# Kernel tuning notes

Measured on AMD Instinct MI355X. Metric: run time of the kernel, lower is better.

## Reference

```python
import jax, jax.numpy as jnp
import numpy as np

D_MODEL = 1024
NUM_HEADS = 16
DEPTH = D_MODEL // NUM_HEADS
B, S = 2, 2048


def setup_inputs() -> dict:
    key = jax.random.key(0)
    ks = jax.random.split(key, 12)
    s = 1.0 / np.sqrt(D_MODEL)
    return {
        "query": jax.random.normal(ks[0], (B, S, D_MODEL), jnp.float32),
        "key": jax.random.normal(ks[1], (B, S, D_MODEL), jnp.float32),
        "value": jax.random.normal(ks[2], (B, S, D_MODEL), jnp.float32),
        "mask": jax.random.randint(ks[3], (B, S), 0, 2, jnp.int32),
        "Wq": jax.random.normal(ks[4], (D_MODEL, D_MODEL), jnp.float32) * s,
        "bq": jnp.zeros((D_MODEL,), jnp.float32),
        "Wk": jax.random.normal(ks[5], (D_MODEL, D_MODEL), jnp.float32) * s,
        "bk": jnp.zeros((D_MODEL,), jnp.float32),
        "Wv": jax.random.normal(ks[6], (D_MODEL, D_MODEL), jnp.float32) * s,
        "bv": jnp.zeros((D_MODEL,), jnp.float32),
        "Wo": jax.random.normal(ks[7], (D_MODEL, D_MODEL), jnp.float32) * s,
        "bo": jnp.zeros((D_MODEL,), jnp.float32),
    }


def _split_heads(x):
    # [B, S, D] -> [B, H, S, depth]
    b, s, _ = x.shape
    return x.reshape(b, s, NUM_HEADS, DEPTH).transpose(0, 2, 1, 3)


def reference(query, key, value, mask, Wq, bq, Wk, bk, Wv, bv, Wo, bo):
    q = _split_heads(query @ Wq.T + bq)
    k = _split_heads(key @ Wk.T + bk)
    v = _split_heads(value @ Wv.T + bv)
    scale = 1.0 / jnp.sqrt(jnp.float32(DEPTH))
    # [B, H, Sq, Sk]
    logits = jnp.einsum("bhqd,bhkd->bhqk", q, k) * scale
    logits = logits + mask.astype(logits.dtype)[:, None, None, :] * (-1e9)
    attn = jax.nn.softmax(logits, axis=-1)
    out = jnp.einsum("bhqk,bhkd->bhqd", attn, v)
    out = out.transpose(0, 2, 1, 3).reshape(query.shape[0], -1, D_MODEL)
    return out @ Wo.T + bo
```

## Files before the change

### kernel.cpp

```cpp
#include <hip/hip_runtime.h>

typedef _Float16 half8 __attribute__((ext_vector_type(8)));
typedef float floatx4 __attribute__((ext_vector_type(4)));

#define D_MODEL 1024
#define NHEAD   16
#define DH      64
#define BATCH   2
#define SEQ     2048
#define M_TOT   4096

#define GLD_LDS16(g, l)                                                          \
  __builtin_amdgcn_global_load_lds(                                              \
      (const __attribute__((address_space(1))) void*)(g),                        \
      (__attribute__((address_space(3))) void*)(l), 16, 0, 0)

__global__ __launch_bounds__(256) void cvt_all(const float* __restrict__ q,
                                               const float* __restrict__ k,
                                               const float* __restrict__ v,
                                               const float* __restrict__ wq,
                                               const float* __restrict__ wk,
                                               const float* __restrict__ wv,
                                               const float* __restrict__ wo,
                                               _Float16* __restrict__ Xall,
                                               _Float16* __restrict__ Wall) {
  int bid = blockIdx.x;
  const float* src;
  _Float16* dst;
  if (bid < 6144) {
    int tsr = bid >> 11;
    src = (tsr == 0) ? q : (tsr == 1) ? k : v;
    dst = Xall + (size_t)tsr * 4194304;
    bid &= 2047;
  } else {
    int w = (bid - 6144) >> 9;
    src = (w == 0) ? wq : (w == 1) ? wk : (w == 2) ? wv : wo;
    dst = Wall + (size_t)w * 1048576;
    bid = (bid - 6144) & 511;
  }
  int off = bid * 2048 + threadIdx.x * 8;
  float4 a = *(const float4*)(src + off);
  float4 b = *(const float4*)(src + off + 4);
  half8 h;
  h[0] = (_Float16)a.x; h[1] = (_Float16)a.y; h[2] = (_Float16)a.z; h[3] = (_Float16)a.w;
  h[4] = (_Float16)b.x; h[5] = (_Float16)b.y; h[6] = (_Float16)b.z; h[7] = (_Float16)b.w;
  *(half8*)(dst + off) = h;
}

__global__ __launch_bounds__(256) void gemm_qkv(const _Float16* __restrict__ Xall,
                                                const _Float16* __restrict__ Wall,
                                                const float* __restrict__ bq,
                                                const float* __restrict__ bk,
                                                const float* __restrict__ bv,
                                                _Float16* __restrict__ Obase) {
  __shared__ alignas(16) _Float16 As[128][32];
  __shared__ alignas(16) _Float16 Bs[128][32];

  const int z = blockIdx.z;
  const _Float16* X = Xall + (size_t)z * 4194304;
  const _Float16* W = Wall + (size_t)z * 1048576;
  const float* bias = (z == 0) ? bq : (z == 1) ? bk : bv;
  _Float16* out = Obase + (size_t)z * 4194304;

  const int t = threadIdx.x, lane = t & 63, wave = t >> 6;
  const int wr = wave >> 1, wc = wave & 1;
  const int m0 = blockIdx.y * 128, n0 = blockIdx.x * 128;
  const int fr = lane & 15, fc = (lane >> 4) * 8, rg = (lane >> 4) * 4;

  floatx4 acc[4][4];
  for (int i = 0; i < 4; i++)
    for (int j = 0; j < 4; j++) acc[i][j] = (floatx4){0.f, 0.f, 0.f, 0.f};

  const int srow = lane >> 2, scol = (lane & 3) * 8;
  const _Float16* gA0 = X + (size_t)(m0 + wave * 32 + srow) * 1024 + scol;
  const _Float16* gA1 = gA0 + 16 * 1024;
  const _Float16* gB0 = W + (size_t)(n0 + wave * 32 + srow) * 1024 + scol;
  const _Float16* gB1 = gB0 + 16 * 1024;
  _Float16* lA0 = &As[wave * 32][0];
  _Float16* lA1 = &As[wave * 32 + 16][0];
  _Float16* lB0 = &Bs[wave * 32][0];
  _Float16* lB1 = &Bs[wave * 32 + 16][0];

  for (int k0 = 0; k0 < 1024; k0 += 32) {
    GLD_LDS16(gA0 + k0, lA0);
    GLD_LDS16(gA1 + k0, lA1);
    GLD_LDS16(gB0 + k0, lB0);
    GLD_LDS16(gB1 + k0, lB1);
    __syncthreads();

    half8 af[4], bw[4];
    for (int i = 0; i < 4; i++) {
      af[i] = *(const half8*)&As[wr * 64 + i * 16 + fr][fc];
      bw[i] = *(const half8*)&Bs[wc * 64 + i * 16 + fr][fc];
    }
    for (int i = 0; i < 4; i++)
      for (int j = 0; j < 4; j++)
        acc[i][j] = __builtin_amdgcn_mfma_f32_16x16x32_f16(af[i], bw[j], acc[i][j], 0, 0, 0);
    __syncthreads();
  }

  for (int i = 0; i < 4; i++)
    for (int j = 0; j < 4; j++) {
      int n = n0 + wc * 64 + j * 16 + fr;
      float bv2 = bias[n];
      int hh = n >> 6, d = n & 63;
      for (int r = 0; r < 4; r++) {
        int m = m0 + wr * 64 + i * 16 + rg + r;
        int bb = m >> 11, s = m & 2047;
        out[(((size_t)(bb * NHEAD + hh)) * SEQ + s) * DH + d] =
            (_Float16)(acc[i][j][r] + bv2);
      }
    }
}

__global__ __launch_bounds__(256) void gemm_wo(const _Float16* __restrict__ ctx,
                                               const _Float16* __restrict__ W,
                                               const float* __restrict__ bias,
                                               float* __restrict__ out) {
  __shared__ alignas(16) _Float16 As[128][32];
  __shared__ alignas(16) _Float16 Bs[64][32];

  const int t = threadIdx.x, lane = t & 63, wave = t >> 6;
  const int m0 = blockIdx.y * 128, n0 = blockIdx.x * 64;
  const int fr = lane & 15, fc = (lane >> 4) * 8, rg = (lane >> 4) * 4;

  floatx4 acc[2][4];
  for (int i = 0; i < 2; i++)
    for (int j = 0; j < 4; j++) acc[i][j] = (floatx4){0.f, 0.f, 0.f, 0.f};

  const int srow = lane >> 2, scol = (lane & 3) * 8;
  const _Float16* gA0 = ctx + (size_t)(m0 + wave * 32 + srow) * 1024 + scol;
  const _Float16* gA1 = gA0 + 16 * 1024;
  const _Float16* gB0 = W + (size_t)(n0 + wave * 16 + srow) * 1024 + scol;
  _Float16* lA0 = &As[wave * 32][0];
  _Float16* lA1 = &As[wave * 32 + 16][0];
  _Float16* lB0 = &Bs[wave * 16][0];

  for (int k0 = 0; k0 < 1024; k0 += 32) {
    GLD_LDS16(gA0 + k0, lA0);
    GLD_LDS16(gA1 + k0, lA1);
    GLD_LDS16(gB0 + k0, lB0);
    __syncthreads();

    half8 af[2], bw[4];
    for (int i = 0; i < 2; i++)
      af[i] = *(const half8*)&As[wave * 32 + i * 16 + fr][fc];
    for (int j = 0; j < 4; j++)
      bw[j] = *(const half8*)&Bs[j * 16 + fr][fc];
    for (int i = 0; i < 2; i++)
      for (int j = 0; j < 4; j++)
        acc[i][j] = __builtin_amdgcn_mfma_f32_16x16x32_f16(af[i], bw[j], acc[i][j], 0, 0, 0);
    __syncthreads();
  }

  for (int i = 0; i < 2; i++)
    for (int j = 0; j < 4; j++) {
      int n = n0 + j * 16 + fr;
      float bv2 = bias[n];
      for (int r = 0; r < 4; r++) {
        int m = m0 + wave * 32 + i * 16 + rg + r;
        out[(size_t)m * D_MODEL + n] = acc[i][j][r] + bv2;
      }
    }
}

__global__ __launch_bounds__(256) void attn_kernel(const _Float16* __restrict__ Qp,
                                                   const _Float16* __restrict__ Kp,
                                                   const _Float16* __restrict__ Vp,
                                                   const int* __restrict__ mask,
                                                   _Float16* __restrict__ ctx) {
  __shared__ alignas(16) char lds[18432 + 34816 + 512];
  _Float16 (*Qs)[72]  = (_Float16(*)[72])lds;
  _Float16 (*Vt)[136] = (_Float16(*)[136])lds;
  _Float16 (*Ks)[72]  = (_Float16(*)[72])(lds + 18432);
  _Float16 (*Ps)[136] = (_Float16(*)[136])(lds + 18432);
  float* Ms = (float*)(lds + 18432 + 34816);

  const int b = blockIdx.z, h = blockIdx.y, q0 = blockIdx.x * 128;
  const int t = threadIdx.x, lane = t & 63, wave = t >> 6;
  const int fr = lane & 15, fc = (lane >> 4) * 8, rg = (lane >> 4) * 4;

  const _Float16* Qg = Qp + ((size_t)(b * NHEAD + h) * SEQ + q0) * DH;
  const _Float16* Kg = Kp + (size_t)(b * NHEAD + h) * SEQ * DH;
  const _Float16* Vg = Vp + (size_t)(b * NHEAD + h) * SEQ * DH;

  {
    int r = t >> 1, c0 = (t & 1) * 32;
    const half8* g = (const half8*)(Qg + r * 64 + c0);
    for (int u = 0; u < 4; u++)
      *(half8*)&Qs[r][c0 + u * 8] = g[u];
  }
  __syncthreads();
  half8 qf[2][2];
  for (int mi = 0; mi < 2; mi++)
    for (int kk = 0; kk < 2; kk++)
      qf[mi][kk] = *(const half8*)&Qs[wave * 32 + mi * 16 + fr][kk * 32 + fc];
  __syncthreads();

  float mrow[2][4], lrow[2][4];
  floatx4 oacc[2][4];
  for (int mi = 0; mi < 2; mi++)
    for (int r = 0; r < 4; r++) { mrow[mi][r] = -3.0e38f; lrow[mi][r] = 0.f; }
  for (int mi = 0; mi < 2; mi++)
    for (int dj = 0; dj < 4; dj++) oacc[mi][dj] = (floatx4){0.f, 0.f, 0.f, 0.f};

  for (int kt = 0; kt < SEQ / 128; kt++) {
    const int k0 = kt * 128;
    {
      int r = t >> 1, c0 = (t & 1) * 32;
      const half8* gk = (const half8*)(Kg + (k0 + r) * 64 + c0);
      for (int u = 0; u < 4; u++)
        *(half8*)&Ks[r][c0 + u * 8] = gk[u];
      const half8* gv = (const half8*)(Vg + (k0 + r) * 64 + c0);
      half8 vv[4];
      for (int u = 0; u < 4; u++) vv[u] = gv[u];
      for (int u = 0; u < 4; u++)
        for (int j = 0; j < 8; j++) Vt[c0 + u * 8 + j][r] = vv[u][j];
      if (t < 128) Ms[t] = (float)mask[b * SEQ + k0 + t] * -1.0e9f;
    }
    __syncthreads();

    floatx4 sa[2][8];
    for (int mi = 0; mi < 2; mi++)
      for (int nj = 0; nj < 8; nj++) sa[mi][nj] = (floatx4){0.f, 0.f, 0.f, 0.f};
    for (int nj = 0; nj < 8; nj++)
      for (int kk = 0; kk < 2; kk++) {
        half8 kf = *(const half8*)&Ks[nj * 16 + fr][kk * 32 + fc];
        sa[0][nj] = __builtin_amdgcn_mfma_f32_16x16x32_f16(qf[0][kk], kf, sa[0][nj], 0, 0, 0);
        sa[1][nj] = __builtin_amdgcn_mfma_f32_16x16x32_f16(qf[1][kk], kf, sa[1][nj], 0, 0, 0);
      }
    __syncthreads();

    for (int nj = 0; nj < 8; nj++) {
      float mk = Ms[nj * 16 + fr];
      for (int mi = 0; mi < 2; mi++)
        for (int r = 0; r < 4; r++)
          sa[mi][nj][r] = sa[mi][nj][r] * 0.125f + mk;
    }

    for (int mi = 0; mi < 2; mi++) {
      for (int r = 0; r < 4; r++) {
        float tm = sa[mi][0][r];
        for (int nj = 1; nj < 8; nj++) tm = fmaxf(tm, sa[mi][nj][r]);
        for (int off = 1; off < 16; off <<= 1) tm = fmaxf(tm, __shfl_xor(tm, off));
        float mnew = fmaxf(mrow[mi][r], tm);
        float alpha = __expf(mrow[mi][r] - mnew);
        mrow[mi][r] = mnew;
        float rs = 0.f;
        for (int nj = 0; nj < 8; nj++) {
          float p = __expf(sa[mi][nj][r] - mnew);
          sa[mi][nj][r] = p;
          rs += p;
        }
        for (int off = 1; off < 16; off <<= 1) rs += __shfl_xor(rs, off);
        lrow[mi][r] = lrow[mi][r] * alpha + rs;
        for (int dj = 0; dj < 4; dj++) oacc[mi][dj][r] *= alpha;
      }
    }

    for (int mi = 0; mi < 2; mi++)
      for (int nj = 0; nj < 8; nj++)
        for (int r = 0; r < 4; r++)
          Ps[wave * 32 + mi * 16 + rg + r][nj * 16 + fr] = (_Float16)sa[mi][nj][r];
    __syncthreads();

    for (int kk = 0; kk < 4; kk++) {
      half8 pf[2], vf[4];
      for (int mi = 0; mi < 2; mi++)
        pf[mi] = *(const half8*)&Ps[wave * 32 + mi * 16 + fr][kk * 32 + fc];
      for (int dj = 0; dj < 4; dj++)
        vf[dj] = *(const half8*)&Vt[dj * 16 + fr][kk * 32 + fc];
      for (int mi = 0; mi < 2; mi++)
        for (int dj = 0; dj < 4; dj++)
          oacc[mi][dj] = __builtin_amdgcn_mfma_f32_16x16x32_f16(pf[mi], vf[dj], oacc[mi][dj], 0, 0, 0);
    }
    __syncthreads();
  }

  for (int mi = 0; mi < 2; mi++)
    for (int r = 0; r < 4; r++) {
      float inv = 1.0f / lrow[mi][r];
      int qrow = q0 + wave * 32 + mi * 16 + rg + r;
      _Float16* o = ctx + ((size_t)b * SEQ + qrow) * D_MODEL + h * DH;
      for (int dj = 0; dj < 4; dj++)
        o[dj * 16 + fr] = (_Float16)(oacc[mi][dj][r] * inv);
    }
}

extern "C" void kernel_launch(void* const* d_in, const int* in_sizes, int n_in,
                              void* d_out, int out_size, void* d_ws, size_t ws_size,
                              hipStream_t stream) {
  const float* query = (const float*)d_in[0];
  const float* key   = (const float*)d_in[1];
  const float* value = (const float*)d_in[2];
  const int*   mask  = (const int*)d_in[3];
  const float* Wq = (const float*)d_in[4];
  const float* bq = (const float*)d_in[5];
  const float* Wk = (const float*)d_in[6];
  const float* bk = (const float*)d_in[7];
  const float* Wv = (const float*)d_in[8];
  const float* bv = (const float*)d_in[9];
  const float* Wo = (const float*)d_in[10];
  const float* bo = (const float*)d_in[11];

  char* ws = (char*)d_ws;
  _Float16* Xall = (_Float16*)(ws);
  _Float16* Wall = (_Float16*)(ws + (size_t)24 * 1024 * 1024);
  _Float16* Qp   = (_Float16*)(ws + (size_t)32 * 1024 * 1024);
  _Float16* ctx  = (_Float16*)(ws + (size_t)56 * 1024 * 1024);

  _Float16* Kp = Qp + (size_t)4194304;
  _Float16* Vp = Qp + (size_t)8388608;

  cvt_all<<<8192, 256, 0, stream>>>(query, key, value, Wq, Wk, Wv, Wo, Xall, Wall);

  gemm_qkv<<<dim3(8, 32, 3), 256, 0, stream>>>(Xall, Wall, bq, bk, bv, Qp);

  attn_kernel<<<dim3(SEQ / 128, NHEAD, BATCH), 256, 0, stream>>>(Qp, Kp, Vp, mask, ctx);

  gemm_wo<<<dim3(16, 32), 256, 0, stream>>>(ctx, Wall + (size_t)3 * 1048576, bo, (float*)d_out);
}
```

Before: 282.5 us.

## Write V pre-transposed from QKV GEMM and load Q fragments directly

The QKV GEMM epilogue for V now stages tiles in shared memory and writes V in a [B,H,DH,SEQ] transposed layout with vectorized stores. The attention kernel can then load V^T tiles with 16-byte copies instead of scattering elements into a transposed LDS tile on every key block. Q fragments are also read straight from global memory, which removes the Q staging buffer and two barriers. The cost is extra LDS traffic and barriers in the V GEMM epilogue.

```diff
diff --git a/kernel.cpp b/kernel.cpp
--- a/kernel.cpp
+++ b/kernel.cpp
@@ -53,8 +53,10 @@
                                                 const float* __restrict__ bk,
                                                 const float* __restrict__ bv,
                                                 _Float16* __restrict__ Obase) {
-  __shared__ alignas(16) _Float16 As[128][32];
-  __shared__ alignas(16) _Float16 Bs[128][32];
+  __shared__ alignas(16) char smem[17408];
+  _Float16 (*As)[32]  = (_Float16(*)[32])smem;
+  _Float16 (*Bs)[32]  = (_Float16(*)[32])(smem + 8192);
+  _Float16 (*Ts)[136] = (_Float16(*)[136])smem;
 
   const int z = blockIdx.z;
   const _Float16* X = Xall + (size_t)z * 4194304;
@@ -99,18 +101,40 @@
     __syncthreads();
   }
 
-  for (int i = 0; i < 4; i++)
-    for (int j = 0; j < 4; j++) {
-      int n = n0 + wc * 64 + j * 16 + fr;
-      float bv2 = bias[n];
-      int hh = n >> 6, d = n & 63;
-      for (int r = 0; r < 4; r++) {
-        int m = m0 + wr * 64 + i * 16 + rg + r;
-        int bb = m >> 11, s = m & 2047;
-        out[(((size_t)(bb * NHEAD + hh)) * SEQ + s) * DH + d] =
-            (_Float16)(acc[i][j][r] + bv2);
-      }
-    }
+  if (z != 2) {
+    for (int i = 0; i < 4; i++)
+      for (int j = 0; j < 4; j++) {
+        int n = n0 + wc * 64 + j * 16 + fr;
+        float bv2 = bias[n];
+        int hh = n >> 6, d = n & 63;
+        for (int r = 0; r < 4; r++) {
+          int m = m0 + wr * 64 + i * 16 + rg + r;
+          int bb = m >> 11, s = m & 2047;
+          out[(((size_t)(bb * NHEAD + hh)) * SEQ + s) * DH + d] =
+              (_Float16)(acc[i][j][r] + bv2);
+        }
+      }
+  } else {
+    const int bb = m0 >> 11, s0 = m0 & 2047;
+    for (int p = 0; p < 2; p++) {
+      __syncthreads();
+      if (wc == p) {
+        for (int j = 0; j < 4; j++) {
+          float bv2 = bias[n0 + p * 64 + j * 16 + fr];
+          for (int i = 0; i < 4; i++)
+            for (int r = 0; r < 4; r++)
+              Ts[j * 16 + fr][wr * 64 + i * 16 + rg + r] =
+                  (_Float16)(acc[i][j][r] + bv2);
+        }
+      }
+      __syncthreads();
+      int dd = t >> 2, c4 = (t & 3) * 32;
+      int hh = (n0 >> 6) + p;
+      _Float16* dst = out + (((size_t)(bb * NHEAD + hh)) * DH + dd) * SEQ + s0;
+      for (int u = 0; u < 4; u++)
+        *(half8*)(dst + c4 + u * 8) = *(const half8*)&Ts[dd][c4 + u * 8];
+    }
+  }
 }
 
 __global__ __launch_bounds__(256) void gemm_wo(const _Float16* __restrict__ ctx,
@@ -166,36 +190,29 @@
 
 __global__ __launch_bounds__(256) void attn_kernel(const _Float16* __restrict__ Qp,
                                                    const _Float16* __restrict__ Kp,
-                                                   const _Float16* __restrict__ Vp,
+                                                   const _Float16* __restrict__ VT,
                                                    const int* __restrict__ mask,
                                                    _Float16* __restrict__ ctx) {
-  __shared__ alignas(16) char lds[18432 + 34816 + 512];
-  _Float16 (*Qs)[72]  = (_Float16(*)[72])lds;
+  __shared__ alignas(16) char lds[17408 + 34816 + 512];
   _Float16 (*Vt)[136] = (_Float16(*)[136])lds;
-  _Float16 (*Ks)[72]  = (_Float16(*)[72])(lds + 18432);
-  _Float16 (*Ps)[136] = (_Float16(*)[136])(lds + 18432);
-  float* Ms = (float*)(lds + 18432 + 34816);
+  _Float16 (*Ks)[72]  = (_Float16(*)[72])(lds + 17408);
+  _Float16 (*Ps)[136] = (_Float16(*)[136])(lds + 17408);
+  float* Ms = (float*)(lds + 17408 + 34816);
 
   const int b = blockIdx.z, h = blockIdx.y, q0 = blockIdx.x * 128;
   const int t = threadIdx.x, lane = t & 63, wave = t >> 6;
   const int fr = lane & 15, fc = (lane >> 4) * 8, rg = (lane >> 4) * 4;
 
-  const _Float16* Qg = Qp + ((size_t)(b * NHEAD + h) * SEQ + q0) * DH;
-  const _Float16* Kg = Kp + (size_t)(b * NHEAD + h) * SEQ * DH;
-  const _Float16* Vg = Vp + (size_t)(b * NHEAD + h) * SEQ * DH;
-
+  const _Float16* Kg  = Kp + (size_t)(b * NHEAD + h) * SEQ * DH;
+  const _Float16* VTg = VT + (size_t)(b * NHEAD + h) * DH * SEQ;
+
+  half8 qf[2][2];
   {
-    int r = t >> 1, c0 = (t & 1) * 32;
-    const half8* g = (const half8*)(Qg + r * 64 + c0);
-    for (int u = 0; u < 4; u++)
-      *(half8*)&Qs[r][c0 + u * 8] = g[u];
-  }
-  __syncthreads();
-  half8 qf[2][2];
-  for (int mi = 0; mi < 2; mi++)
-    for (int kk = 0; kk < 2; kk++)
-      qf[mi][kk] = *(const half8*)&Qs[wave * 32 + mi * 16 + fr][kk * 32 + fc];
-  __syncthreads();
+    const _Float16* Qgw = Qp + ((size_t)(b * NHEAD + h) * SEQ + q0 + wave * 32) * DH;
+    for (int mi = 0; mi < 2; mi++)
+      for (int kk = 0; kk < 2; kk++)
+        qf[mi][kk] = *(const half8*)(Qgw + (mi * 16 + fr) * DH + kk * 32 + fc);
+  }
 
   float mrow[2][4], lrow[2][4];
   floatx4 oacc[2][4];
@@ -211,11 +228,10 @@
       const half8* gk = (const half8*)(Kg + (k0 + r) * 64 + c0);
       for (int u = 0; u < 4; u++)
         *(half8*)&Ks[r][c0 + u * 8] = gk[u];
-      const half8* gv = (const half8*)(Vg + (k0 + r) * 64 + c0);
-      half8 vv[4];
-      for (int u = 0; u < 4; u++) vv[u] = gv[u];
+      int dd = t >> 2, c4 = (t & 3) * 32;
+      const _Float16* gv = VTg + (size_t)dd * SEQ + k0 + c4;
       for (int u = 0; u < 4; u++)
-        for (int j = 0; j < 8; j++) Vt[c0 + u * 8 + j][r] = vv[u][j];
+        *(half8*)&Vt[dd][c4 + u * 8] = *(const half8*)(gv + u * 8);
       if (t < 128) Ms[t] = (float)mask[b * SEQ + k0 + t] * -1.0e9f;
     }
     __syncthreads();
@@ -310,13 +326,13 @@
   _Float16* ctx  = (_Float16*)(ws + (size_t)56 * 1024 * 1024);
 
   _Float16* Kp = Qp + (size_t)4194304;
-  _Float16* Vp = Qp + (size_t)8388608;
+  _Float16* VT = Qp + (size_t)8388608;
 
   cvt_all<<<8192, 256, 0, stream>>>(query, key, value, Wq, Wk, Wv, Wo, Xall, Wall);
 
   gemm_qkv<<<dim3(8, 32, 3), 256, 0, stream>>>(Xall, Wall, bq, bk, bv, Qp);
 
-  attn_kernel<<<dim3(SEQ / 128, NHEAD, BATCH), 256, 0, stream>>>(Qp, Kp, Vp, mask, ctx);
+  attn_kernel<<<dim3(SEQ / 128, NHEAD, BATCH), 256, 0, stream>>>(Qp, Kp, VT, mask, ctx);
 
   gemm_wo<<<dim3(16, 32), 256, 0, stream>>>(ctx, Wall + (size_t)3 * 1048576, bo, (float*)d_out);
 }
```

Result: no change. 285.3 us (+1.0%).
